# Kernel optimization log

Hardware: AMD Instinct MI355X
Metric: run time of the kernel (lower is better)

## Reference

```python
import jax, jax.numpy as jnp
import numpy as np

N_NODES = 100000
DIM = 64
N_EDGES = 1250000
NR_LAYERS = 1
EPS = 1e-12  # F.normalize default eps


def setup_inputs() -> dict:
    key = jax.random.key(0)
    k1, k2, k3 = jax.random.split(key, 3)
    x = jax.random.normal(k1, (N_NODES, DIM), dtype=jnp.float32)
    edge_index = jax.random.randint(k2, (2, N_EDGES), 0, N_NODES, dtype=jnp.int64 if jax.config.jax_enable_x64 else jnp.int32)
    edge_weights = jax.random.uniform(k3, (N_EDGES, 1), dtype=jnp.float32)
    return {"x": x, "edge_index": edge_index, "edge_weights": edge_weights}


def _scatter_mean(x, src, dst, n_nodes):
    # gather source features along edges, mean-reduce onto destination nodes
    sums = jax.ops.segment_sum(x[src], dst, num_segments=n_nodes)  # [N, D]
    cnt = jax.ops.segment_sum(jnp.ones((src.shape[0],), x.dtype), dst, num_segments=n_nodes)
    return sums / jnp.maximum(cnt, 1.0)[:, None]


def _layer(x, src, dst):
    # Faithful to source: update() overwrites the linear output with
    # F.normalize(aggr_out); out_f == out_b since new_edge_index == edge_index.
    agg = _scatter_mean(x, src, dst, x.shape[0])  # [N, D]
    norm = jnp.linalg.norm(agg, axis=1, keepdims=True)
    h = agg / jnp.maximum(norm, EPS)
    return 2.0 * h  # out_f + out_b


def reference(x, edge_index, edge_weights):
    src = edge_index[0]
    dst = edge_index[1]
    for _ in range(NR_LAYERS):
        x = _layer(x, src, dst)
        x = jax.nn.relu(x)
    return x
```

## Files before the change

kernel.cpp:

```cpp
#include <hip/hip_runtime.h>

#define N_NODES 100000
#define DIM 64
#define N_EDGES 1250000
#define EPS 1e-12f

#define PART 128
#define NP ((N_NODES + PART - 1) / PART)
#define SLOT 2048
#define CSTRIDE 16
#define CH 4096
#define NCH ((N_EDGES + CH - 1) / CH)
#define BT 512
#define EPT (CH / BT)
#define NCV ((N_NODES * DIM / 8 + BT - 1) / BT)

typedef unsigned short ushort8 __attribute__((ext_vector_type(8)));

__device__ inline unsigned short f2bf(float f) {
    unsigned int u = __float_as_uint(f);
    return (unsigned short)((u + 0x7FFFu + ((u >> 16) & 1u)) >> 16);
}
__device__ inline float bf2f(unsigned short h) {
    return __uint_as_float(((unsigned int)h) << 16);
}

__global__ __launch_bounds__(BT)
void convert_bucket_kernel(const float4* __restrict__ x4,
                           ushort8* __restrict__ xh8,
                           const int* __restrict__ src,
                           const int* __restrict__ dst,
                           int* __restrict__ pcursor,
                           int* __restrict__ ebuf) {
    __shared__ int hist[NP];
    __shared__ int lstart[NP];
    __shared__ int cur[NP];
    __shared__ int gb[NP];
    __shared__ int sorted[CH];
    __shared__ unsigned short pb[CH];
    __shared__ int wsum[BT / 64];

    int t = threadIdx.x;

    if (blockIdx.x >= NCH) {
        int i = (blockIdx.x - NCH) * BT + t;
        if (i < N_NODES * DIM / 8) {
            float4 a = x4[2 * i];
            float4 b = x4[2 * i + 1];
            ushort8 o;
            o[0] = f2bf(a.x); o[1] = f2bf(a.y); o[2] = f2bf(a.z); o[3] = f2bf(a.w);
            o[4] = f2bf(b.x); o[5] = f2bf(b.y); o[6] = f2bf(b.z); o[7] = f2bf(b.w);
            xh8[i] = o;
        }
        return;
    }

    int e0 = blockIdx.x * CH;
    for (int p = t; p < NP; p += BT) hist[p] = 0;
    __syncthreads();

    int d[EPT];
    #pragma unroll
    for (int i = 0; i < EPT; ++i) {
        int e = e0 + i * BT + t;
        d[i] = (e < N_EDGES) ? dst[e] : -1;
        if (d[i] >= 0) atomicAdd(&hist[d[i] >> 7], 1);
    }
    __syncthreads();

    for (int p = t; p < NP; p += BT) {
        int c = hist[p];
        gb[p] = c ? atomicAdd(&pcursor[p * CSTRIDE], c) : 0;
    }

    int lane = t & 63, w = t >> 6;
    int b0 = 2 * t, b1 = 2 * t + 1;
    int c0 = (b0 < NP) ? hist[b0] : 0;
    int c1 = (b1 < NP) ? hist[b1] : 0;
    int ms = c0 + c1;
    int v = ms;
    #pragma unroll
    for (int off = 1; off < 64; off <<= 1) {
        int u = __shfl_up(v, off, 64);
        if (lane >= off) v += u;
    }
    if (lane == 63) wsum[w] = v;
    __syncthreads();
    if (t == 0) {
        int run = 0;
        #pragma unroll
        for (int i = 0; i < BT / 64; ++i) { int c = wsum[i]; wsum[i] = run; run += c; }
    }
    __syncthreads();
    int excl = wsum[w] + v - ms;
    if (b0 < NP) { lstart[b0] = excl;      cur[b0] = excl; }
    if (b1 < NP) { lstart[b1] = excl + c0; cur[b1] = excl + c0; }
    __syncthreads();

    #pragma unroll
    for (int i = 0; i < EPT; ++i) {
        if (d[i] >= 0) {
            int e = e0 + i * BT + t;
            int p = d[i] >> 7;
            int pos = atomicAdd(&cur[p], 1);
            sorted[pos] = (src[e] << 7) | (d[i] & 127);
            pb[pos] = (unsigned short)p;
        }
    }
    __syncthreads();

    int vcnt = min(CH, N_EDGES - e0);
    for (int i = t; i < vcnt; i += BT) {
        int pk = sorted[i];
        int p = pb[i];
        ebuf[p * SLOT + gb[p] + (i - lstart[p])] = pk;
    }
}

__global__ __launch_bounds__(BT, 8)
void aggregate_kernel(const ushort8* __restrict__ xh8,
                      const int* __restrict__ pcursor,
                      const int* __restrict__ ebuf,
                      float* __restrict__ out) {
    __shared__ int lraw[SLOT];
    __shared__ int lcsr[SLOT];
    __shared__ int lhist[PART];
    __shared__ int lcur[PART];
    __shared__ int bridge;
    int p = blockIdx.x;
    int t = threadIdx.x;
    int lane = t & 63, w = t >> 6;
    int n = lane >> 3, sub = lane & 7;

    if (t < PART) lhist[t] = 0;
    __syncthreads();

    int cnt = pcursor[p * CSTRIDE];
    const int* __restrict__ eb = ebuf + p * SLOT;
    for (int i = t; i < cnt; i += BT) {
        int pk = eb[i];
        lraw[i] = pk;
        atomicAdd(&lhist[pk & 127], 1);
    }
    __syncthreads();

    int myc = 0, vincl = 0;
    if (t < PART) {
        myc = lhist[t];
        vincl = myc;
        #pragma unroll
        for (int off = 1; off < 64; off <<= 1) {
            int u = __shfl_up(vincl, off, 64);
            if (lane >= off) vincl += u;
        }
        if (t == 63) bridge = vincl;
    }
    __syncthreads();
    if (t < PART) {
        int add = (t >= 64) ? bridge : 0;
        lhist[t] = vincl + add;
        lcur[t]  = vincl + add - myc;
    }
    __syncthreads();

    for (int i = t; i < cnt; i += BT) {
        int pk = lraw[i];
        int pos = atomicAdd(&lcur[pk & 127], 1);
        lcsr[pos] = pk >> 7;
    }
    __syncthreads();

    #pragma unroll
    for (int q = 0; q < 2; ++q) {
        int nl = q * 64 + w * 8 + n;
        int gnode = p * PART + nl;
        int beg = nl ? lhist[nl - 1] : 0;
        int dn  = lhist[nl] - beg;

        float acc[8] = {0.f,0.f,0.f,0.f,0.f,0.f,0.f,0.f};
        for (int e = 0; e < dn; e += 8) {
            #pragma unroll
            for (int i = 0; i < 8; ++i) {
                if (e + i < dn) {
                    int s = lcsr[beg + e + i];
                    ushort8 vv = xh8[(size_t)s * 8 + sub];
                    #pragma unroll
                    for (int k = 0; k < 8; ++k) acc[k] += bf2f(vv[k]);
                }
            }
        }

        float ss = 0.f;
        #pragma unroll
        for (int k = 0; k < 8; ++k) ss += acc[k] * acc[k];
        ss += __shfl_xor(ss, 1, 64);
        ss += __shfl_xor(ss, 2, 64);
        ss += __shfl_xor(ss, 4, 64);

        float scale = 2.0f / fmaxf(sqrtf(ss), EPS);
        if (gnode < N_NODES) {
            float4 o0, o1;
            o0.x = fmaxf(acc[0] * scale, 0.f); o0.y = fmaxf(acc[1] * scale, 0.f);
            o0.z = fmaxf(acc[2] * scale, 0.f); o0.w = fmaxf(acc[3] * scale, 0.f);
            o1.x = fmaxf(acc[4] * scale, 0.f); o1.y = fmaxf(acc[5] * scale, 0.f);
            o1.z = fmaxf(acc[6] * scale, 0.f); o1.w = fmaxf(acc[7] * scale, 0.f);
            ((float4*)out)[(size_t)gnode * 16 + 2 * sub]     = o0;
            ((float4*)out)[(size_t)gnode * 16 + 2 * sub + 1] = o1;
        }
    }
}

extern "C" void kernel_launch(void* const* d_in, const int* in_sizes, int n_in,
                              void* d_out, int out_size, void* d_ws, size_t ws_size,
                              hipStream_t stream) {
    const float* x  = (const float*)d_in[0];
    const int*   ei = (const int*)d_in[1];
    float* out = (float*)d_out;

    const int* src = ei;
    const int* dst = ei + N_EDGES;

    ushort8* xh  = (ushort8*)d_ws;
    int* pcursor = (int*)((char*)d_ws + (size_t)N_NODES * DIM * 2);
    int* ebuf    = pcursor + NP * CSTRIDE;

    hipMemsetAsync(pcursor, 0, NP * CSTRIDE * sizeof(int), stream);

    convert_bucket_kernel<<<NCH + NCV, BT, 0, stream>>>(
        (const float4*)x, xh, src, dst, pcursor, ebuf);

    aggregate_kernel<<<NP, BT, 0, stream>>>(xh, pcursor, ebuf, out);
}
```

Baseline: 133.5 us.

## Group edges by source-node chunk so all blocks gather from the same region together

The aggregate kernel now builds a local CSR sorted by (source chunk, destination node), with 7 chunks of 16384 source nodes each. Every block then walks the chunks in the same order, so blocks running at the same time gather from the same ~2 MB slice of the bf16 feature table, which should improve L2 hit rate. In exchange, per-node loops are split into 7 short segments with more loop overhead, and the histogram and scan grow from 128 to 896 bins.

```diff
diff --git a/kernel.cpp b/kernel.cpp
--- a/kernel.cpp
+++ b/kernel.cpp
@@ -14,6 +14,10 @@
 #define BT 512
 #define EPT (CH / BT)
 #define NCV ((N_NODES * DIM / 8 + BT - 1) / BT)
+
+#define CBITS 14
+#define NCHK 7
+#define NBIN (NCHK * PART)
 
 typedef unsigned short ushort8 __attribute__((ext_vector_type(8)));
 
@@ -124,15 +128,15 @@
                       float* __restrict__ out) {
     __shared__ int lraw[SLOT];
     __shared__ int lcsr[SLOT];
-    __shared__ int lhist[PART];
-    __shared__ int lcur[PART];
-    __shared__ int bridge;
+    __shared__ int lhist[NBIN];
+    __shared__ int lcur[NBIN];
+    __shared__ int wsum[BT / 64];
     int p = blockIdx.x;
     int t = threadIdx.x;
     int lane = t & 63, w = t >> 6;
     int n = lane >> 3, sub = lane & 7;
 
-    if (t < PART) lhist[t] = 0;
+    for (int i = t; i < NBIN; i += BT) lhist[i] = 0;
     __syncthreads();
 
     int cnt = pcursor[p * CSTRIDE];
@@ -140,59 +144,71 @@
     for (int i = t; i < cnt; i += BT) {
         int pk = eb[i];
         lraw[i] = pk;
-        atomicAdd(&lhist[pk & 127], 1);
-    }
-    __syncthreads();
-
-    int myc = 0, vincl = 0;
-    if (t < PART) {
-        myc = lhist[t];
-        vincl = myc;
-        #pragma unroll
-        for (int off = 1; off < 64; off <<= 1) {
-            int u = __shfl_up(vincl, off, 64);
-            if (lane >= off) vincl += u;
-        }
-        if (t == 63) bridge = vincl;
-    }
-    __syncthreads();
-    if (t < PART) {
-        int add = (t >= 64) ? bridge : 0;
-        lhist[t] = vincl + add;
-        lcur[t]  = vincl + add - myc;
-    }
+        atomicAdd(&lhist[((pk >> (7 + CBITS)) << 7) | (pk & 127)], 1);
+    }
+    __syncthreads();
+
+    int b0 = 2 * t, b1 = 2 * t + 1;
+    int c0 = (b0 < NBIN) ? lhist[b0] : 0;
+    int c1 = (b1 < NBIN) ? lhist[b1] : 0;
+    int ms = c0 + c1;
+    int v = ms;
+    #pragma unroll
+    for (int off = 1; off < 64; off <<= 1) {
+        int u = __shfl_up(v, off, 64);
+        if (lane >= off) v += u;
+    }
+    if (lane == 63) wsum[w] = v;
+    __syncthreads();
+    if (t == 0) {
+        int run = 0;
+        #pragma unroll
+        for (int i = 0; i < BT / 64; ++i) { int c = wsum[i]; wsum[i] = run; run += c; }
+    }
+    __syncthreads();
+    int excl = wsum[w] + v - ms;
+    if (b0 < NBIN) { lhist[b0] = excl + c0;      lcur[b0] = excl; }
+    if (b1 < NBIN) { lhist[b1] = excl + c0 + c1; lcur[b1] = excl + c0; }
     __syncthreads();
 
     for (int i = t; i < cnt; i += BT) {
         int pk = lraw[i];
-        int pos = atomicAdd(&lcur[pk & 127], 1);
+        int bin = ((pk >> (7 + CBITS)) << 7) | (pk & 127);
+        int pos = atomicAdd(&lcur[bin], 1);
         lcsr[pos] = pk >> 7;
     }
     __syncthreads();
+
+    float acc[2][8] = {{0.f,0.f,0.f,0.f,0.f,0.f,0.f,0.f},
+                       {0.f,0.f,0.f,0.f,0.f,0.f,0.f,0.f}};
+    for (int c = 0; c < NCHK; ++c) {
+        #pragma unroll
+        for (int q = 0; q < 2; ++q) {
+            int nl = q * 64 + w * 8 + n;
+            int bin = c * PART + nl;
+            int beg = bin ? lhist[bin - 1] : 0;
+            int end = lhist[bin];
+            for (int e = beg; e < end; e += 4) {
+                #pragma unroll
+                for (int i = 0; i < 4; ++i) {
+                    if (e + i < end) {
+                        int s = lcsr[e + i];
+                        ushort8 vv = xh8[(size_t)s * 8 + sub];
+                        #pragma unroll
+                        for (int k = 0; k < 8; ++k) acc[q][k] += bf2f(vv[k]);
+                    }
+                }
+            }
+        }
+    }
 
     #pragma unroll
     for (int q = 0; q < 2; ++q) {
         int nl = q * 64 + w * 8 + n;
         int gnode = p * PART + nl;
-        int beg = nl ? lhist[nl - 1] : 0;
-        int dn  = lhist[nl] - beg;
-
-        float acc[8] = {0.f,0.f,0.f,0.f,0.f,0.f,0.f,0.f};
-        for (int e = 0; e < dn; e += 8) {
-            #pragma unroll
-            for (int i = 0; i < 8; ++i) {
-                if (e + i < dn) {
-                    int s = lcsr[beg + e + i];
-                    ushort8 vv = xh8[(size_t)s * 8 + sub];
-                    #pragma unroll
-                    for (int k = 0; k < 8; ++k) acc[k] += bf2f(vv[k]);
-                }
-            }
-        }
-
         float ss = 0.f;
         #pragma unroll
-        for (int k = 0; k < 8; ++k) ss += acc[k] * acc[k];
+        for (int k = 0; k < 8; ++k) ss += acc[q][k] * acc[q][k];
         ss += __shfl_xor(ss, 1, 64);
         ss += __shfl_xor(ss, 2, 64);
         ss += __shfl_xor(ss, 4, 64);
@@ -200,10 +216,10 @@
         float scale = 2.0f / fmaxf(sqrtf(ss), EPS);
         if (gnode < N_NODES) {
             float4 o0, o1;
-            o0.x = fmaxf(acc[0] * scale, 0.f); o0.y = fmaxf(acc[1] * scale, 0.f);
-            o0.z = fmaxf(acc[2] * scale, 0.f); o0.w = fmaxf(acc[3] * scale, 0.f);
-            o1.x = fmaxf(acc[4] * scale, 0.f); o1.y = fmaxf(acc[5] * scale, 0.f);
-            o1.z = fmaxf(acc[6] * scale, 0.f); o1.w = fmaxf(acc[7] * scale, 0.f);
+            o0.x = fmaxf(acc[q][0] * scale, 0.f); o0.y = fmaxf(acc[q][1] * scale, 0.f);
+            o0.z = fmaxf(acc[q][2] * scale, 0.f); o0.w = fmaxf(acc[q][3] * scale, 0.f);
+            o1.x = fmaxf(acc[q][4] * scale, 0.f); o1.y = fmaxf(acc[q][5] * scale, 0.f);
+            o1.z = fmaxf(acc[q][6] * scale, 0.f); o1.w = fmaxf(acc[q][7] * scale, 0.f);
             ((float4*)out)[(size_t)gnode * 16 + 2 * sub]     = o0;
             ((float4*)out)[(size_t)gnode * 16 + 2 * sub + 1] = o1;
         }
```

Result: slower. 140.4 us (+5.2%).
